# Optimization experiments

Hardware: AMD Instinct MI355X
Metric: run time of the kernel (lower is better)

The kernel has to match this reference:

```python
import jax, jax.numpy as jnp
import numpy as np


def setup_inputs() -> dict:
    key = jax.random.key(0)
    k1, k2, k3 = jax.random.split(key, 3)
    B, C, D = 4096, 10000, 512
    feat = jax.random.normal(k1, (B, D), dtype=jnp.float32)
    label = jax.random.randint(k2, (B,), 0, C, dtype=jnp.int64)
    # xavier_uniform for weights [C, D]: bound = sqrt(6/(C+D))
    bound = np.sqrt(6.0 / (C + D)).astype(np.float32)
    weights = jax.random.uniform(k3, (C, D), dtype=jnp.float32, minval=-bound, maxval=bound)
    return {"feat": feat, "label": label, "weights": weights}


def reference(feat, label, weights):
    # pairwise squared L2 distance between feat [B,D] and weights [C,D]
    # computed via the Gram-matrix identity (same math as broadcast-sub-square-sum)
    f2 = jnp.sum(feat * feat, axis=-1, keepdims=True)          # [B,1]
    w2 = jnp.sum(weights * weights, axis=-1)[None, :]          # [1,C]
    cross = jnp.einsum('bd,cd->bc', feat, weights)             # [B,C]
    metric = jnp.maximum(f2 + w2 - 2.0 * cross, 0.0)           # [B,C] sq dists
    kernal_metric = jnp.exp(-0.01 * metric)                    # RBF kernel logits
    # original computes avg kernel value at true labels but then overrides
    # scale = 1.0, so logits are just the kernel values
    scale = 1.0
    train_logits = scale * kernal_metric
    valuation_logits = scale * kernal_metric
    return (train_logits, valuation_logits, weights)
```

## Files before the change

### kernel.cpp

```cpp
#include <hip/hip_runtime.h>
#include <hip/hip_bf16.h>
#include <stdint.h>

#define BDIM 4096
#define CDIM 10000
#define DDIM 512
#define CPAD 10112
#define NTILES 2528
#define GRID 512
#define STRIDE_TILE (2 * 128 * DDIM)

typedef __bf16 bf16_t;
typedef __attribute__((ext_vector_type(2))) __bf16 bf16x2;
typedef __attribute__((ext_vector_type(8))) __bf16 bf16x8;
typedef __attribute__((ext_vector_type(2))) float f32x2;
typedef __attribute__((ext_vector_type(4))) float f32x4;

__device__ __forceinline__ void gl_lds16(const void* g, void* s) {
  __builtin_amdgcn_global_load_lds(
      (const __attribute__((address_space(1))) void*)g,
      (__attribute__((address_space(3))) void*)s, 16, 0, 0);
}

__global__ __launch_bounds__(256) void prep(
    const float* __restrict__ feat, const float* __restrict__ w,
    bf16_t* __restrict__ fb, bf16_t* __restrict__ wb,
    float* __restrict__ f2, float* __restrict__ w2,
    float* __restrict__ wout) {
  const int b = blockIdx.x;
  const int t = threadIdx.x;
  __shared__ float red[4];
  if (b < BDIM) {
    const f32x2 v = ((const f32x2*)(feat + (size_t)b * DDIM))[t];
    bf16x2 o;
    o.x = (__bf16)v.x;
    o.y = (__bf16)v.y;
    ((bf16x2*)fb)[(size_t)b * (DDIM / 2) + t] = o;
    float ss = v.x * v.x + v.y * v.y;
#pragma unroll
    for (int off = 32; off > 0; off >>= 1) ss += __shfl_down(ss, off);
    if ((t & 63) == 0) red[t >> 6] = ss;
    __syncthreads();
    if (t == 0) f2[b] = red[0] + red[1] + red[2] + red[3];
  } else {
    const int row = b - BDIM;
    if (row < CDIM) {
      const f32x2 v = ((const f32x2*)(w + (size_t)row * DDIM))[t];
      __builtin_nontemporal_store(v, (f32x2*)(wout + (size_t)row * DDIM) + t);
      bf16x2 o;
      o.x = (__bf16)v.x;
      o.y = (__bf16)v.y;
      ((bf16x2*)wb)[(size_t)row * (DDIM / 2) + t] = o;
      float ss = v.x * v.x + v.y * v.y;
#pragma unroll
      for (int off = 32; off > 0; off >>= 1) ss += __shfl_down(ss, off);
      if ((t & 63) == 0) red[t >> 6] = ss;
      __syncthreads();
      if (t == 0) w2[row] = red[0] + red[1] + red[2] + red[3];
    } else {
      bf16x2 z;
      z.x = (__bf16)0.0f;
      z.y = (__bf16)0.0f;
      ((bf16x2*)wb)[(size_t)row * (DDIM / 2) + t] = z;
      if (t == 0) w2[row] = 0.0f;
    }
  }
}

__global__ __launch_bounds__(256, 2) void rbf_gemm(
    const bf16_t* __restrict__ A,
    const bf16_t* __restrict__ Bw,
    const float* __restrict__ f2g, const float* __restrict__ w2g,
    float* __restrict__ out) {
  __shared__ __align__(16) bf16_t stg[3 * 8192];
  __shared__ __align__(16) float sbuf[2][8][132];
  __shared__ float w2all[5][128];

  const int b = blockIdx.x;
  const int t = threadIdx.x;
  const int lane = t & 63;
  const int wv = t >> 6;
  const int wm = (wv >> 1) * 64;
  const int wn = (wv & 1) * 64;
  const int fr = lane & 15;
  const int k8 = (lane >> 4) * 8;
  const int c_l = (lane >> 4) * 4;

  const int wg0 = (b & 7) * 316 + (b >> 3);
  const int bm = wg0 & 31;
  const int bn0 = wg0 >> 5;
  const int s_total = (NTILES - 1 - b) / GRID + 1;

  float f2r[4];
#pragma unroll
  for (int mi = 0; mi < 4; ++mi)
    f2r[mi] = f2g[bm * 128 + wm + mi * 16 + fr];
  for (int s_ = 0; s_ < s_total; ++s_)
    if (t < 128) w2all[s_][t] = w2g[(bn0 + 2 * s_) * 128 + t];

  const int sr = t >> 2;
  const int sc = (t & 3) * 8;
  const bf16_t* ga0 = A + (size_t)(bm * 128 + sr) * DDIM + sc;
  const bf16_t* ga1 = ga0 + (size_t)64 * DDIM;
  const bf16_t* gb_cur = Bw + (size_t)(bn0 * 128 + sr) * DDIM + sc;
  const bf16_t* gb_nxt = gb_cur + (s_total > 1 ? STRIDE_TILE : 0);

#define STAGE(off, ak, bptr, bk)                       \
  do {                                                 \
    gl_lds16(ga0 + (ak), stg + (off) + t * 8);         \
    gl_lds16(ga1 + (ak), stg + (off) + 2048 + t * 8);  \
    gl_lds16((bptr) + (bk), stg + (off) + 4096 + t * 8);          \
    gl_lds16((bptr) + (bk) + (size_t)64 * DDIM,                   \
             stg + (off) + 4096 + 2048 + t * 8);                  \
  } while (0)

#define SLICEW(k)                                                        \
  do {                                                                   \
    if (((wv >> 1) == ((k) >> 3)) && ((fr >> 3) == ((k) & 1))) {         \
      const int row_ = fr & 7;                                           \
      _Pragma("unroll") for (int ni = 0; ni < 4; ++ni)                   \
          *(f32x4*)&sbuf[(k) & 1][row_][wn + ni * 16 + c_l] =            \
              stash[((k) >> 1) & 3][ni];                                 \
    }                                                                    \
  } while (0)

#define DRAIN(k, bnd)                                                    \
  do {                                                                   \
    const int r_ = t >> 5;                                               \
    const int c_ = (t & 31) * 4;                                         \
    const f32x4 v_ = *(const f32x4*)&sbuf[(k) & 1][r_][c_];              \
    const int gcol_ = (bnd) * 128 + c_;                                  \
    if (gcol_ < CDIM) {                                                  \
      float* orow_ =                                                     \
          out + (size_t)(bm * 128 + (k) * 8 + r_) * CDIM + gcol_;        \
      __builtin_nontemporal_store(v_, (f32x4*)orow_);                    \
      __builtin_nontemporal_store(v_, (f32x4*)(orow_ + BC));             \
    }                                                                    \
  } while (0)

  const size_t BC = (size_t)BDIM * CDIM;

  f32x4 acc[4][4];
  f32x4 stash[4][4];
#pragma unroll
  for (int i = 0; i < 4; ++i)
#pragma unroll
    for (int j = 0; j < 4; ++j) acc[i][j] = (f32x4){0.f, 0.f, 0.f, 0.f};

  STAGE(0, 0, gb_cur, 0);
  STAGE(8192, 32, gb_cur, 32);
  __syncthreads();

  int o0 = 0, o1 = 8192, o2 = 16384;
  int bn_dr = bn0;

  for (int s = 0; s < s_total; ++s) {
    const bool hasst = (s > 0);
#pragma unroll
    for (int kt = 0; kt < 16; ++kt) {
      if (hasst && kt >= 1) DRAIN(kt - 1, bn_dr);
      asm volatile("" ::: "memory");
      if (kt <= 13)
        STAGE(o2, ((kt + 2) & 15) * 32, gb_cur, (kt + 2) * 32);
      else
        STAGE(o2, ((kt + 2) & 15) * 32, gb_nxt, ((kt + 2) & 15) * 32);
      asm volatile("" ::: "memory");
      if (hasst) SLICEW(kt);
      {
        const bf16_t* Ab = stg + o0;
        bf16x8 af[4], wf[4];
#pragma unroll
        for (int mi = 0; mi < 4; ++mi)
          af[mi] = *(const bf16x8*)(Ab + (wm + mi * 16 + fr) * 32 + k8);
#pragma unroll
        for (int ni = 0; ni < 4; ++ni)
          wf[ni] = *(const bf16x8*)(Ab + 4096 + (wn + ni * 16 + fr) * 32 + k8);
        __builtin_amdgcn_s_setprio(1);
#pragma unroll
        for (int mi = 0; mi < 4; ++mi)
#pragma unroll
          for (int ni = 0; ni < 4; ++ni)
            acc[mi][ni] = __builtin_amdgcn_mfma_f32_16x16x32_bf16(
                wf[ni], af[mi], acc[mi][ni], 0, 0, 0);
        __builtin_amdgcn_s_setprio(0);
      }
      asm volatile("s_waitcnt vmcnt(4) lgkmcnt(0)" ::: "memory");
      __builtin_amdgcn_s_barrier();
      const int tmp = o0;
      o0 = o1;
      o1 = o2;
      o2 = tmp;
    }
    if (hasst) DRAIN(15, bn_dr);
#pragma unroll
    for (int mi = 0; mi < 4; ++mi) {
      const float fv = f2r[mi];
#pragma unroll
      for (int ni = 0; ni < 4; ++ni) {
        const f32x4 w4 = *(const f32x4*)&w2all[s][wn + ni * 16 + c_l];
        f32x4 st;
#pragma unroll
        for (int j = 0; j < 4; ++j) {
          float m = fv + w4[j] - 2.0f * acc[mi][ni][j];
          m = fmaxf(m, 0.0f);
          st[j] = __expf(-0.01f * m);
        }
        stash[mi][ni] = st;
        acc[mi][ni] = (f32x4){0.f, 0.f, 0.f, 0.f};
      }
    }
    bn_dr = bn0 + 2 * s;
    gb_cur = gb_nxt;
    if (s + 2 < s_total) gb_nxt += STRIDE_TILE;
  }

#pragma unroll
  for (int k = 0; k < 16; ++k) {
    SLICEW(k);
    asm volatile("s_waitcnt lgkmcnt(0)" ::: "memory");
    __builtin_amdgcn_s_barrier();
    DRAIN(k, bn_dr);
  }
#undef STAGE
#undef SLICEW
#undef DRAIN
}

extern "C" void kernel_launch(void* const* d_in, const int* in_sizes, int n_in,
                              void* d_out, int out_size, void* d_ws,
                              size_t ws_size, hipStream_t stream) {
  const float* feat = (const float*)d_in[0];
  const float* w = (const float*)d_in[2];
  float* out = (float*)d_out;

  char* ws = (char*)d_ws;
  bf16_t* fb = (bf16_t*)ws;
  bf16_t* wb = (bf16_t*)(ws + 4194304);
  float* f2 = (float*)(ws + 4194304 + 10354688);
  float* w2 = (float*)(ws + 4194304 + 10354688 + 16384);

  float* wout = out + (size_t)2 * BDIM * CDIM;

  prep<<<BDIM + CPAD, 256, 0, stream>>>(feat, w, fb, wb, f2, w2, wout);
  rbf_gemm<<<GRID, 256, 0, stream>>>(fb, wb, f2, w2, out);
}
```

Baseline: 114.8 us.

## Shrink GEMM tile to 64x128 and double grid for higher occupancy

Result: slower. 150.7 us (+31.3%).

```diff
diff --git a/kernel.cpp b/kernel.cpp
--- a/kernel.cpp
+++ b/kernel.cpp
@@ -6,8 +6,8 @@
 #define CDIM 10000
 #define DDIM 512
 #define CPAD 10112
-#define NTILES 2528
-#define GRID 512
+#define GRID 1024
+#define CHUNK 632
 #define STRIDE_TILE (2 * 128 * DDIM)
 
 typedef __bf16 bf16_t;
@@ -67,124 +67,127 @@
   }
 }
 
-__global__ __launch_bounds__(256, 2) void rbf_gemm(
+__global__ __launch_bounds__(256, 4) void rbf_gemm(
     const bf16_t* __restrict__ A,
     const bf16_t* __restrict__ Bw,
     const float* __restrict__ f2g, const float* __restrict__ w2g,
     float* __restrict__ out) {
-  __shared__ __align__(16) bf16_t stg[3 * 8192];
-  __shared__ __align__(16) float sbuf[2][8][132];
-  __shared__ float w2all[5][128];
+  __shared__ __align__(16) bf16_t stg[3 * 6144];
+  __shared__ __align__(16) float sbuf[2][4][128];
 
   const int b = blockIdx.x;
   const int t = threadIdx.x;
   const int lane = t & 63;
   const int wv = t >> 6;
-  const int wm = (wv >> 1) * 64;
-  const int wn = (wv & 1) * 64;
+  const int wm2 = (wv >> 1) * 32;
+  const int wn2 = (wv & 1) * 64;
   const int fr = lane & 15;
   const int k8 = (lane >> 4) * 8;
   const int c_l = (lane >> 4) * 4;
 
-  const int wg0 = (b & 7) * 316 + (b >> 3);
-  const int bm = wg0 & 31;
-  const int bn0 = wg0 >> 5;
-  const int s_total = (NTILES - 1 - b) / GRID + 1;
-
-  float f2r[4];
-#pragma unroll
-  for (int mi = 0; mi < 4; ++mi)
-    f2r[mi] = f2g[bm * 128 + wm + mi * 16 + fr];
-  for (int s_ = 0; s_ < s_total; ++s_)
-    if (t < 128) w2all[s_][t] = w2g[(bn0 + 2 * s_) * 128 + t];
+  const int off = b >> 3;
+  const int wg0 = (b & 7) * CHUNK + off;
+  const int bm = wg0 & 63;
+  const int bn0 = wg0 >> 6;
+  const int s_total = (CHUNK - 1 - off) / 128 + 1;
+
+  float f2r[2];
+#pragma unroll
+  for (int mi = 0; mi < 2; ++mi)
+    f2r[mi] = f2g[bm * 64 + wm2 + mi * 16 + fr];
 
   const int sr = t >> 2;
   const int sc = (t & 3) * 8;
-  const bf16_t* ga0 = A + (size_t)(bm * 128 + sr) * DDIM + sc;
-  const bf16_t* ga1 = ga0 + (size_t)64 * DDIM;
+  const bf16_t* gaA = A + (size_t)(bm * 64 + sr) * DDIM + sc;
   const bf16_t* gb_cur = Bw + (size_t)(bn0 * 128 + sr) * DDIM + sc;
   const bf16_t* gb_nxt = gb_cur + (s_total > 1 ? STRIDE_TILE : 0);
 
-#define STAGE(off, ak, bptr, bk)                       \
-  do {                                                 \
-    gl_lds16(ga0 + (ak), stg + (off) + t * 8);         \
-    gl_lds16(ga1 + (ak), stg + (off) + 2048 + t * 8);  \
-    gl_lds16((bptr) + (bk), stg + (off) + 4096 + t * 8);          \
-    gl_lds16((bptr) + (bk) + (size_t)64 * DDIM,                   \
-             stg + (off) + 4096 + 2048 + t * 8);                  \
+#define STAGE(o_, ak, bptr, bk)                                        \
+  do {                                                                 \
+    gl_lds16(gaA + (ak), stg + (o_) + t * 8);                          \
+    gl_lds16((bptr) + (bk), stg + (o_) + 2048 + t * 8);                \
+    gl_lds16((bptr) + (bk) + (size_t)64 * DDIM,                        \
+             stg + (o_) + 4096 + t * 8);                               \
   } while (0)
 
-#define SLICEW(k)                                                        \
-  do {                                                                   \
-    if (((wv >> 1) == ((k) >> 3)) && ((fr >> 3) == ((k) & 1))) {         \
-      const int row_ = fr & 7;                                           \
-      _Pragma("unroll") for (int ni = 0; ni < 4; ++ni)                   \
-          *(f32x4*)&sbuf[(k) & 1][row_][wn + ni * 16 + c_l] =            \
-              stash[((k) >> 1) & 3][ni];                                 \
-    }                                                                    \
+#define SLICEW(k)                                                      \
+  do {                                                                 \
+    if (((wv >> 1) == ((k) >> 3)) && ((fr >> 2) == ((k) & 3))) {       \
+      const int row_ = fr & 3;                                         \
+      const int mi_ = ((k) >> 2) & 1;                                  \
+      _Pragma("unroll") for (int ni = 0; ni < 4; ++ni) {               \
+        const int g_ = (wn2 >> 2) + ni * 4 + (lane >> 4);              \
+        const int q_ = (g_ & ~7) | ((g_ + 4 * row_) & 7);              \
+        *(f32x4*)&sbuf[(k) & 1][row_][q_ * 4] = stash[mi_][ni];        \
+      }                                                                \
+    }                                                                  \
   } while (0)
 
-#define DRAIN(k, bnd)                                                    \
-  do {                                                                   \
-    const int r_ = t >> 5;                                               \
-    const int c_ = (t & 31) * 4;                                         \
-    const f32x4 v_ = *(const f32x4*)&sbuf[(k) & 1][r_][c_];              \
-    const int gcol_ = (bnd) * 128 + c_;                                  \
-    if (gcol_ < CDIM) {                                                  \
-      float* orow_ =                                                     \
-          out + (size_t)(bm * 128 + (k) * 8 + r_) * CDIM + gcol_;        \
-      __builtin_nontemporal_store(v_, (f32x4*)orow_);                    \
-      __builtin_nontemporal_store(v_, (f32x4*)(orow_ + BC));             \
-    }                                                                    \
+#define DRAIN(k, bnd)                                                  \
+  do {                                                                 \
+    const int seg_ = t >> 7;                                           \
+    const int u_ = t & 127;                                            \
+    const int r_ = u_ >> 5;                                            \
+    const int g_ = u_ & 31;                                            \
+    const int q_ = (g_ & ~7) | ((g_ + 4 * r_) & 7);                    \
+    const f32x4 v_ = *(const f32x4*)&sbuf[(k) & 1][r_][q_ * 4];        \
+    const int gcol_ = (bnd)*128 + g_ * 4;                              \
+    if (gcol_ < CDIM) {                                                \
+      float* p_ = out + (size_t)(bm * 64 + (k)*4 + r_) * CDIM + gcol_; \
+      if (seg_) p_ += BC;                                              \
+      __builtin_nontemporal_store(v_, (f32x4*)p_);                     \
+    }                                                                  \
   } while (0)
 
   const size_t BC = (size_t)BDIM * CDIM;
 
-  f32x4 acc[4][4];
-  f32x4 stash[4][4];
-#pragma unroll
-  for (int i = 0; i < 4; ++i)
+  f32x4 acc[2][4];
+  f32x4 stash[2][4];
+#pragma unroll
+  for (int i = 0; i < 2; ++i)
 #pragma unroll
     for (int j = 0; j < 4; ++j) acc[i][j] = (f32x4){0.f, 0.f, 0.f, 0.f};
 
   STAGE(0, 0, gb_cur, 0);
-  STAGE(8192, 32, gb_cur, 32);
+  STAGE(6144, 32, gb_cur, 32);
   __syncthreads();
 
-  int o0 = 0, o1 = 8192, o2 = 16384;
+  int o0 = 0, o1 = 6144, o2 = 12288;
   int bn_dr = bn0;
 
   for (int s = 0; s < s_total; ++s) {
     const bool hasst = (s > 0);
+    const int bn = bn0 + 2 * s;
 #pragma unroll
     for (int kt = 0; kt < 16; ++kt) {
-      if (hasst && kt >= 1) DRAIN(kt - 1, bn_dr);
-      asm volatile("" ::: "memory");
       if (kt <= 13)
-        STAGE(o2, ((kt + 2) & 15) * 32, gb_cur, (kt + 2) * 32);
+        STAGE(o2, (kt + 2) * 32, gb_cur, (kt + 2) * 32);
       else
         STAGE(o2, ((kt + 2) & 15) * 32, gb_nxt, ((kt + 2) & 15) * 32);
-      asm volatile("" ::: "memory");
+      if (hasst && kt >= 1) DRAIN(kt - 1, bn_dr);
       if (hasst) SLICEW(kt);
       {
         const bf16_t* Ab = stg + o0;
-        bf16x8 af[4], wf[4];
-#pragma unroll
-        for (int mi = 0; mi < 4; ++mi)
-          af[mi] = *(const bf16x8*)(Ab + (wm + mi * 16 + fr) * 32 + k8);
+        bf16x8 af[2], wf[4];
+#pragma unroll
+        for (int mi = 0; mi < 2; ++mi)
+          af[mi] = *(const bf16x8*)(Ab + (wm2 + mi * 16 + fr) * 32 + k8);
 #pragma unroll
         for (int ni = 0; ni < 4; ++ni)
-          wf[ni] = *(const bf16x8*)(Ab + 4096 + (wn + ni * 16 + fr) * 32 + k8);
+          wf[ni] = *(const bf16x8*)(Ab + 2048 + (wn2 + ni * 16 + fr) * 32 + k8);
         __builtin_amdgcn_s_setprio(1);
 #pragma unroll
-        for (int mi = 0; mi < 4; ++mi)
+        for (int mi = 0; mi < 2; ++mi)
 #pragma unroll
           for (int ni = 0; ni < 4; ++ni)
             acc[mi][ni] = __builtin_amdgcn_mfma_f32_16x16x32_bf16(
                 wf[ni], af[mi], acc[mi][ni], 0, 0, 0);
         __builtin_amdgcn_s_setprio(0);
       }
-      asm volatile("s_waitcnt vmcnt(4) lgkmcnt(0)" ::: "memory");
+      if (hasst)
+        asm volatile("s_waitcnt vmcnt(5) lgkmcnt(0)" ::: "memory");
+      else
+        asm volatile("s_waitcnt vmcnt(3) lgkmcnt(0)" ::: "memory");
       __builtin_amdgcn_s_barrier();
       const int tmp = o0;
       o0 = o1;
@@ -192,16 +195,19 @@
       o2 = tmp;
     }
     if (hasst) DRAIN(15, bn_dr);
-#pragma unroll
-    for (int mi = 0; mi < 4; ++mi) {
+    f32x4 w2v[4];
+#pragma unroll
+    for (int ni = 0; ni < 4; ++ni)
+      w2v[ni] = *(const f32x4*)(w2g + bn * 128 + wn2 + ni * 16 + c_l);
+#pragma unroll
+    for (int mi = 0; mi < 2; ++mi) {
       const float fv = f2r[mi];
 #pragma unroll
       for (int ni = 0; ni < 4; ++ni) {
-        const f32x4 w4 = *(const f32x4*)&w2all[s][wn + ni * 16 + c_l];
         f32x4 st;
 #pragma unroll
         for (int j = 0; j < 4; ++j) {
-          float m = fv + w4[j] - 2.0f * acc[mi][ni][j];
+          float m = fv + w2v[ni][j] - 2.0f * acc[mi][ni][j];
           m = fmaxf(m, 0.0f);
           st[j] = __expf(-0.01f * m);
         }
@@ -209,7 +215,7 @@
         acc[mi][ni] = (f32x4){0.f, 0.f, 0.f, 0.f};
       }
     }
-    bn_dr = bn0 + 2 * s;
+    bn_dr = bn;
     gb_cur = gb_nxt;
     if (s + 2 < s_total) gb_nxt += STRIDE_TILE;
   }
```
